# Kernel tuning notes

Measured on AMD Instinct MI355X. Metric: run time of the kernel, lower is better.

## Reference

```python
import jax, jax.numpy as jnp
import numpy as np
import math

N, E, D, H, L = 50000, 800000, 256, 8, 8
DK = D // H
DFF = 4 * D


def _layernorm(h, g, b, eps=1e-5):
    m = jnp.mean(h, axis=-1, keepdims=True)
    v = jnp.mean((h - m) ** 2, axis=-1, keepdims=True)
    return (h - m) * jax.lax.rsqrt(v + eps) * g + b


def setup_inputs() -> dict:
    key = jax.random.key(0)
    ks = jax.random.split(key, 16)
    s = 1.0 / math.sqrt(D)
    x = jax.random.normal(ks[0], (N, D), dtype=jnp.float32)
    # every node gets >=1 in-edge so z > 0 everywhere (as in real connected graphs)
    edge_src = jax.random.randint(ks[1], (E,), 0, N, dtype=jnp.int32)
    edge_dst = jnp.concatenate([
        jnp.arange(N, dtype=jnp.int32),
        jax.random.randint(ks[2], (E - N,), 0, N, dtype=jnp.int32),
    ])
    return {
        "x": x,
        "edge_src": edge_src,
        "edge_dst": edge_dst,
        "Wq": jax.random.normal(ks[3], (L, D, D), dtype=jnp.float32) * s,
        "bq": jnp.zeros((L, D), dtype=jnp.float32),
        "Wk": jax.random.normal(ks[4], (L, D, D), dtype=jnp.float32) * s,
        "Wv": jax.random.normal(ks[5], (L, D, D), dtype=jnp.float32) * s,
        "Wo": jax.random.normal(ks[6], (L, D, D), dtype=jnp.float32) * s,
        "bo": jnp.zeros((L, D), dtype=jnp.float32),
        "ln1_g": jnp.ones((L, D), dtype=jnp.float32),
        "ln1_b": jnp.zeros((L, D), dtype=jnp.float32),
        "W1": jax.random.normal(ks[7], (L, D, DFF), dtype=jnp.float32) * s,
        "b1": jnp.zeros((L, DFF), dtype=jnp.float32),
        "W2": jax.random.normal(ks[8], (L, DFF, D), dtype=jnp.float32) * (1.0 / math.sqrt(DFF)),
        "b2": jnp.zeros((L, D), dtype=jnp.float32),
        "ln2_g": jnp.ones((L, D), dtype=jnp.float32),
        "ln2_b": jnp.zeros((L, D), dtype=jnp.float32),
    }


def _layer(x, src, dst, Wq, bq, Wk, Wv, Wo, bo, g1, b1n, W1, b1, W2, b2, g2, b2n):
    n = x.shape[0]
    q = (x @ Wq + bq).reshape(n, H, DK)
    k = (x @ Wk).reshape(n, H, DK)
    v = (x @ Wv).reshape(n, H, DK)
    # edge score: src_dot_dst('k','q') -> [E, H]
    score = jnp.einsum('ehd,ehd->eh', k[src], q[dst])
    # scaled_exp: exp(clamp(score / sqrt(d_k), -5, 5))
    score = jnp.exp(jnp.clip(score / math.sqrt(DK), -5.0, 5.0))
    # u_mul_e + sum aggregation -> wv [N, H, DK]; copy_edge + sum -> z [N, H]
    msg = v[src] * score[:, :, None]
    wv = jax.ops.segment_sum(msg, dst, num_segments=n)
    z = jax.ops.segment_sum(score, dst, num_segments=n)
    o = (wv / z[:, :, None]).reshape(n, D)
    h = _layernorm(x + o @ Wo + bo, g1, b1n)
    # FFN with residual + layernorm
    ff = jax.nn.relu(h @ W1 + b1) @ W2 + b2
    return _layernorm(h + ff, g2, b2n)


def reference(x, edge_src, edge_dst, Wq, bq, Wk, Wv, Wo, bo, ln1_g, ln1_b,
              W1, b1, W2, b2, ln2_g, ln2_b):
    for i in range(L):
        x = _layer(x, edge_src, edge_dst, Wq[i], bq[i], Wk[i], Wv[i], Wo[i],
                   bo[i], ln1_g[i], ln1_b[i], W1[i], b1[i], W2[i], b2[i],
                   ln2_g[i], ln2_b[i])
    return x
```

## Files before the change

kernel.cpp:

```cpp
#include <hip/hip_runtime.h>
#include <cstdint>
#include <cstddef>

#define D 256
#define H 8
#define DFF 1024

typedef short s16x8 __attribute__((ext_vector_type(8)));
typedef float f32x4 __attribute__((ext_vector_type(4)));

static inline int cdiv(int a, int b) { return (a + b - 1) / b; }

__device__ inline uint16_t f2bf(float x) {
    unsigned u = __float_as_uint(x);
    u += 0x7FFFu + ((u >> 16) & 1u);
    return (uint16_t)(u >> 16);
}
__device__ inline float bf2f(uint16_t h) {
    return __uint_as_float(((unsigned)h) << 16);
}

__device__ inline void gload_lds16(const void* g, void* l) {
    __builtin_amdgcn_global_load_lds(
        (const __attribute__((address_space(1))) void*)g,
        (__attribute__((address_space(3))) void*)l, 16, 0, 0);
}

__global__ __launch_bounds__(256) void zero_int_kernel(int* __restrict__ p, int count)
{
    int i = blockIdx.x * blockDim.x + threadIdx.x;
    if (i < count) p[i] = 0;
}

__global__ __launch_bounds__(256) void count_deg_kernel(
    const int* __restrict__ edst, int* __restrict__ deg, int E)
{
    int e = blockIdx.x * blockDim.x + threadIdx.x;
    if (e < E) atomicAdd(&deg[edst[e]], 1);
}

__global__ __launch_bounds__(256) void block_sum_kernel(
    const int* __restrict__ deg, int* __restrict__ bsum, int N)
{
    int t = threadIdx.x;
    int gid = blockIdx.x * 256 + t;
    int val = (gid < N) ? deg[gid] : 0;
    #pragma unroll
    for (int o = 1; o < 64; o <<= 1) val += __shfl_xor(val, o);
    __shared__ int r[4];
    if ((t & 63) == 0) r[t >> 6] = val;
    __syncthreads();
    if (t == 0) bsum[blockIdx.x] = r[0] + r[1] + r[2] + r[3];
}

__global__ __launch_bounds__(256) void scan_bsum_kernel(int* __restrict__ bsum, int nb)
{
    __shared__ int tmp[256];
    int t = threadIdx.x;
    int val = (t < nb) ? bsum[t] : 0;
    tmp[t] = val;
    __syncthreads();
    for (int off = 1; off < 256; off <<= 1) {
        int add = (t >= off) ? tmp[t - off] : 0;
        __syncthreads();
        tmp[t] += add;
        __syncthreads();
    }
    if (t < nb) bsum[t] = tmp[t] - val;
}

__global__ __launch_bounds__(256) void scan_write_kernel(
    const int* __restrict__ deg, const int* __restrict__ bsum,
    int* __restrict__ rowptr, int* __restrict__ cursor, int N)
{
    __shared__ int tmp[256];
    int t = threadIdx.x;
    int gid = blockIdx.x * 256 + t;
    int val = (gid < N) ? deg[gid] : 0;
    tmp[t] = val;
    __syncthreads();
    for (int off = 1; off < 256; off <<= 1) {
        int add = (t >= off) ? tmp[t - off] : 0;
        __syncthreads();
        tmp[t] += add;
        __syncthreads();
    }
    int excl = tmp[t] - val + bsum[blockIdx.x];
    if (gid < N) { rowptr[gid] = excl; cursor[gid] = excl; }
    if (gid == N - 1) rowptr[N] = excl + val;
}

__global__ __launch_bounds__(256) void fill_csr_kernel(
    const int* __restrict__ esrc, const int* __restrict__ edst,
    int* __restrict__ cursor, int* __restrict__ csr_src, int E)
{
    int e = blockIdx.x * blockDim.x + threadIdx.x;
    if (e < E) {
        int pos = atomicAdd(&cursor[edst[e]], 1);
        csr_src[pos] = esrc[e];
    }
}

__global__ __launch_bounds__(256) void transpose_cast_kernel(
    const float* __restrict__ in, uint16_t* __restrict__ out,
    int R, int C, size_t inLS, size_t outLS)
{
    __shared__ float t[32][33];
    in  += blockIdx.z * inLS;
    out += blockIdx.z * outLS;
    int c0 = blockIdx.x * 32, r0 = blockIdx.y * 32;
    int tx = threadIdx.x, ty = threadIdx.y;
    #pragma unroll
    for (int i = 0; i < 4; ++i)
        t[ty + i * 8][tx] = in[(size_t)(r0 + ty + i * 8) * C + c0 + tx];
    __syncthreads();
    #pragma unroll
    for (int i = 0; i < 4; ++i)
        out[(size_t)(c0 + ty + i * 8) * R + r0 + tx] = f2bf(t[tx][ty + i * 8]);
}

__global__ __launch_bounds__(256) void cast_f32_bf16_kernel(
    const float* __restrict__ in, uint16_t* __restrict__ out, int n4)
{
    int i = blockIdx.x * blockDim.x + threadIdx.x;
    if (i >= n4) return;
    float4 f = ((const float4*)in)[i];
    uint16_t o0 = f2bf(f.x), o1 = f2bf(f.y), o2 = f2bf(f.z), o3 = f2bf(f.w);
    uint2 pk;
    pk.x = (unsigned)o0 | ((unsigned)o1 << 16);
    pk.y = (unsigned)o2 | ((unsigned)o3 << 16);
    ((uint2*)out)[i] = pk;
}

__global__ __launch_bounds__(256) void build_qkv_bias_kernel(
    const float* __restrict__ bq, float* __restrict__ qb, int total)
{
    int i = blockIdx.x * blockDim.x + threadIdx.x;
    if (i >= total) return;
    int l = i / 768, c = i - l * 768;
    qb[i] = (c < 256) ? bq[l * 256 + c] : 0.f;
}

__global__ __launch_bounds__(256) void gemm_bf16_kernel(
    const uint16_t* __restrict__ A, int lda, int M, int K,
    const uint16_t* __restrict__ BT, int Nc,
    const float* __restrict__ bias,
    uint16_t* __restrict__ Cb, int relu)
{
    __shared__ __align__(16) uint16_t As[128 * 32];
    __shared__ __align__(16) uint16_t Bs[128 * 32];

    const int tid  = threadIdx.x;
    const int lane = tid & 63;
    const int w    = tid >> 6;
    const int wr   = w >> 1, wc = w & 1;
    const int quad = lane >> 4;
    const int l15  = lane & 15;

    const int m0 = blockIdx.x * 128;
    const int n0 = blockIdx.y * 128;

    f32x4 acc[4][4] = {};

    const int jbase = w * 2;
    const int srow  = lane >> 2;
    const int skc   = (lane & 3) * 8;

    for (int k0 = 0; k0 < K; k0 += 32) {
        #pragma unroll
        for (int jj = 0; jj < 2; ++jj) {
            int j = jbase + jj;
            int r = j * 16 + srow;
            int gr = m0 + r; if (gr > M - 1) gr = M - 1;
            gload_lds16(A  + (size_t)gr * lda + k0 + skc, &As[j * 512]);
            gload_lds16(BT + (size_t)(n0 + r) * K + k0 + skc, &Bs[j * 512]);
        }
        __syncthreads();

        s16x8 af[4], bf[4];
        #pragma unroll
        for (int t = 0; t < 4; ++t) {
            af[t] = *(const s16x8*)&As[(wr * 64 + t * 16 + l15) * 32 + quad * 8];
            bf[t] = *(const s16x8*)&Bs[(wc * 64 + t * 16 + l15) * 32 + quad * 8];
        }
        #pragma unroll
        for (int i = 0; i < 4; ++i)
            #pragma unroll
            for (int jt = 0; jt < 4; ++jt)
                acc[i][jt] = __builtin_amdgcn_mfma_f32_16x16x32_bf16(
                    af[i], bf[jt], acc[i][jt], 0, 0, 0);
        __syncthreads();
    }

    float bv[4];
    #pragma unroll
    for (int jt = 0; jt < 4; ++jt)
        bv[jt] = bias ? bias[n0 + wc * 64 + jt * 16 + l15] : 0.f;

    #pragma unroll
    for (int i = 0; i < 4; ++i) {
        #pragma unroll
        for (int r = 0; r < 4; ++r) {
            int m = m0 + wr * 64 + i * 16 + quad * 4 + r;
            if (m >= M) continue;
            #pragma unroll
            for (int jt = 0; jt < 4; ++jt) {
                int n = n0 + wc * 64 + jt * 16 + l15;
                float val = acc[i][jt][r] + bv[jt];
                if (relu) val = fmaxf(val, 0.f);
                Cb[(size_t)m * Nc + n] = f2bf(val);
            }
        }
    }
}

__global__ __launch_bounds__(256) void gemm_ln_kernel(
    const uint16_t* __restrict__ A, int lda, int M, int K,
    const uint16_t* __restrict__ BT,
    const float* __restrict__ bias,
    const float* __restrict__ resid,
    const float* __restrict__ g, const float* __restrict__ b,
    float* __restrict__ Cf, uint16_t* __restrict__ Cb)
{
    __shared__ __align__(16) uint16_t As[64 * 32];
    __shared__ __align__(16) uint16_t Bs[256 * 32];
    __shared__ float sS[64][4];
    __shared__ float sQ[64][4];

    const int tid  = threadIdx.x;
    const int lane = tid & 63;
    const int w    = tid >> 6;
    const int quad = lane >> 4;
    const int l15  = lane & 15;

    const int m0 = blockIdx.x * 64;

    f32x4 acc[4][4] = {};

    for (int k0 = 0; k0 < K; k0 += 32) {
        {
            int slot = tid;
            int r = slot >> 2, kc = (slot & 3) * 8;
            int gr = m0 + r; if (gr > M - 1) gr = M - 1;
            gload_lds16(A + (size_t)gr * lda + k0 + kc, &As[slot * 8]);
        }
        #pragma unroll
        for (int i = 0; i < 4; ++i) {
            int slot = i * 256 + tid;
            int n = slot >> 2, kc = (slot & 3) * 8;
            gload_lds16(BT + (size_t)n * K + k0 + kc, &Bs[slot * 8]);
        }
        __syncthreads();

        s16x8 af[4], bf[4];
        #pragma unroll
        for (int t = 0; t < 4; ++t) {
            af[t] = *(const s16x8*)&As[(t * 16 + l15) * 32 + quad * 8];
            bf[t] = *(const s16x8*)&Bs[(w * 64 + t * 16 + l15) * 32 + quad * 8];
        }
        #pragma unroll
        for (int i = 0; i < 4; ++i)
            #pragma unroll
            for (int jt = 0; jt < 4; ++jt)
                acc[i][jt] = __builtin_amdgcn_mfma_f32_16x16x32_bf16(
                    af[i], bf[jt], acc[i][jt], 0, 0, 0);
        __syncthreads();
    }

    float bv[4], gv[4], bbv[4];
    #pragma unroll
    for (int jt = 0; jt < 4; ++jt) {
        int n = w * 64 + jt * 16 + l15;
        bv[jt]  = bias[n];
        gv[jt]  = g[n];
        bbv[jt] = b[n];
    }

    #pragma unroll
    for (int i = 0; i < 4; ++i) {
        #pragma unroll
        for (int r = 0; r < 4; ++r) {
            int ml = i * 16 + quad * 4 + r;
            int m  = m0 + ml;
            bool valid = (m < M);
            float s = 0.f, s2 = 0.f;
            #pragma unroll
            for (int jt = 0; jt < 4; ++jt) {
                int n = w * 64 + jt * 16 + l15;
                float val = acc[i][jt][r] + bv[jt];
                if (valid) val += resid[(size_t)m * 256 + n];
                acc[i][jt][r] = val;
                s += val;
                s2 += val * val;
            }
            #pragma unroll
            for (int o = 1; o < 16; o <<= 1) {
                s  += __shfl_xor(s, o);
                s2 += __shfl_xor(s2, o);
            }
            if (l15 == 0) { sS[ml][w] = s; sQ[ml][w] = s2; }
        }
    }
    __syncthreads();

    #pragma unroll
    for (int i = 0; i < 4; ++i) {
        #pragma unroll
        for (int r = 0; r < 4; ++r) {
            int ml = i * 16 + quad * 4 + r;
            int m  = m0 + ml;
            if (m >= M) continue;
            float s  = sS[ml][0] + sS[ml][1] + sS[ml][2] + sS[ml][3];
            float s2 = sQ[ml][0] + sQ[ml][1] + sQ[ml][2] + sQ[ml][3];
            float mean = s * (1.f / 256.f);
            float var  = s2 * (1.f / 256.f) - mean * mean;
            float rstd = rsqrtf(var + 1e-5f);
            #pragma unroll
            for (int jt = 0; jt < 4; ++jt) {
                int n = w * 64 + jt * 16 + l15;
                float out = (acc[i][jt][r] - mean) * rstd * gv[jt] + bbv[jt];
                Cf[(size_t)m * 256 + n] = out;
                if (Cb) Cb[(size_t)m * 256 + n] = f2bf(out);
            }
        }
    }
}

__global__ __launch_bounds__(256) void node_attn_kernel(
    uint16_t* __restrict__ qkv,
    const int* __restrict__ rowptr, const int* __restrict__ csr_src, int N)
{
    int node = (blockIdx.x * blockDim.x + threadIdx.x) >> 6;
    int lane = threadIdx.x & 63;
    if (node >= N) return;

    uint16_t* qp = qkv + (size_t)node * 768 + lane * 4;
    uint2 qu = *(const uint2*)qp;
    float q0 = bf2f((uint16_t)(qu.x & 0xFFFF)), q1 = bf2f((uint16_t)(qu.x >> 16));
    float q2 = bf2f((uint16_t)(qu.y & 0xFFFF)), q3 = bf2f((uint16_t)(qu.y >> 16));

    float a0 = 0.f, a1 = 0.f, a2 = 0.f, a3 = 0.f, zacc = 0.f;
    const float inv_sqrt_dk = 0.17677669529663687f;

    int beg = rowptr[node], end = rowptr[node + 1];
    int i = beg;
    for (; i + 1 < end; i += 2) {
        int s0 = csr_src[i], s1 = csr_src[i + 1];
        const uint16_t* b0 = qkv + (size_t)s0 * 768;
        const uint16_t* b1 = qkv + (size_t)s1 * 768;
        uint2 ku0 = *(const uint2*)(b0 + 256 + lane * 4);
        uint2 ku1 = *(const uint2*)(b1 + 256 + lane * 4);
        uint2 vu0 = *(const uint2*)(b0 + 512 + lane * 4);
        uint2 vu1 = *(const uint2*)(b1 + 512 + lane * 4);

        float p0 = bf2f((uint16_t)(ku0.x & 0xFFFF)) * q0
                 + bf2f((uint16_t)(ku0.x >> 16))   * q1
                 + bf2f((uint16_t)(ku0.y & 0xFFFF)) * q2
                 + bf2f((uint16_t)(ku0.y >> 16))   * q3;
        float p1 = bf2f((uint16_t)(ku1.x & 0xFFFF)) * q0
                 + bf2f((uint16_t)(ku1.x >> 16))   * q1
                 + bf2f((uint16_t)(ku1.y & 0xFFFF)) * q2
                 + bf2f((uint16_t)(ku1.y >> 16))   * q3;
        p0 += __shfl_xor(p0, 1); p1 += __shfl_xor(p1, 1);
        p0 += __shfl_xor(p0, 2); p1 += __shfl_xor(p1, 2);
        p0 += __shfl_xor(p0, 4); p1 += __shfl_xor(p1, 4);
        float sc0 = __expf(fminf(fmaxf(p0 * inv_sqrt_dk, -5.f), 5.f));
        float sc1 = __expf(fminf(fmaxf(p1 * inv_sqrt_dk, -5.f), 5.f));

        a0 += bf2f((uint16_t)(vu0.x & 0xFFFF)) * sc0;
        a1 += bf2f((uint16_t)(vu0.x >> 16))   * sc0;
        a2 += bf2f((uint16_t)(vu0.y & 0xFFFF)) * sc0;
        a3 += bf2f((uint16_t)(vu0.y >> 16))   * sc0;
        zacc += sc0;
        a0 += bf2f((uint16_t)(vu1.x & 0xFFFF)) * sc1;
        a1 += bf2f((uint16_t)(vu1.x >> 16))   * sc1;
        a2 += bf2f((uint16_t)(vu1.y & 0xFFFF)) * sc1;
        a3 += bf2f((uint16_t)(vu1.y >> 16))   * sc1;
        zacc += sc1;
    }
    if (i < end) {
        int s = csr_src[i];
        const uint16_t* base = qkv + (size_t)s * 768;
        uint2 ku = *(const uint2*)(base + 256 + lane * 4);
        float p = bf2f((uint16_t)(ku.x & 0xFFFF)) * q0
                + bf2f((uint16_t)(ku.x >> 16))   * q1
                + bf2f((uint16_t)(ku.y & 0xFFFF)) * q2
                + bf2f((uint16_t)(ku.y >> 16))   * q3;
        p += __shfl_xor(p, 1);
        p += __shfl_xor(p, 2);
        p += __shfl_xor(p, 4);
        float sc = __expf(fminf(fmaxf(p * inv_sqrt_dk, -5.f), 5.f));
        uint2 vu = *(const uint2*)(base + 512 + lane * 4);
        a0 += bf2f((uint16_t)(vu.x & 0xFFFF)) * sc;
        a1 += bf2f((uint16_t)(vu.x >> 16))   * sc;
        a2 += bf2f((uint16_t)(vu.y & 0xFFFF)) * sc;
        a3 += bf2f((uint16_t)(vu.y >> 16))   * sc;
        zacc += sc;
    }
    float inv = 1.f / zacc;
    uint2 pk;
    pk.x = (unsigned)f2bf(a0 * inv) | ((unsigned)f2bf(a1 * inv) << 16);
    pk.y = (unsigned)f2bf(a2 * inv) | ((unsigned)f2bf(a3 * inv) << 16);
    *(uint2*)qp = pk;
}

extern "C" void kernel_launch(void* const* d_in, const int* in_sizes, int n_in,
                              void* d_out, int out_size, void* d_ws, size_t ws_size,
                              hipStream_t stream)
{
    const float* x0   = (const float*)d_in[0];
    const int* esrc   = (const int*)d_in[1];
    const int* edst   = (const int*)d_in[2];
    const float* Wq   = (const float*)d_in[3];
    const float* bq   = (const float*)d_in[4];
    const float* Wk   = (const float*)d_in[5];
    const float* Wv   = (const float*)d_in[6];
    const float* Wo   = (const float*)d_in[7];
    const float* bo   = (const float*)d_in[8];
    const float* ln1g = (const float*)d_in[9];
    const float* ln1b = (const float*)d_in[10];
    const float* W1   = (const float*)d_in[11];
    const float* b1   = (const float*)d_in[12];
    const float* W2   = (const float*)d_in[13];
    const float* b2   = (const float*)d_in[14];
    const float* ln2g = (const float*)d_in[15];
    const float* ln2b = (const float*)d_in[16];

    const int N = in_sizes[0] / D;
    const int E = in_sizes[1];
    const int L = in_sizes[3] / (D * D);
    const size_t ND = (size_t)N * D;

    char* p = (char*)d_ws;
    float* bufX = (float*)p;         p += ND * 4;
    uint16_t* xb  = (uint16_t*)p;
    uint16_t* t1  = xb;              p += ND * 2;
    uint16_t* qkv = (uint16_t*)p;    p += (size_t)N * 768 * 2;
    uint16_t* hb  = (uint16_t*)p;    p += ND * 2;
    uint16_t* BTqkv = (uint16_t*)p;  p += (size_t)L * 768 * 256 * 2;
    uint16_t* BTo   = (uint16_t*)p;  p += (size_t)L * 256 * 256 * 2;
    uint16_t* BT1   = (uint16_t*)p;  p += (size_t)L * 1024 * 256 * 2;
    uint16_t* BT2   = (uint16_t*)p;  p += (size_t)L * 256 * 1024 * 2;
    float* qbias    = (float*)p;     p += (size_t)L * 768 * 4;
    int* rowptr  = (int*)p;          p += (size_t)(N + 1) * 4;
    int* cursor  = (int*)p;          p += (size_t)N * 4;
    int* deg     = cursor;
    int* csr_src = (int*)p;          p += (size_t)E * 4;
    int* bsum    = (int*)p;

    const int nb = cdiv(N, 256);
    dim3 blk(256);
    int edgeBlocks = cdiv(E, 256);
    int nodeBlocks = cdiv(N, 4);

    dim3 tb(32, 8);
    transpose_cast_kernel<<<dim3(8, 8, L), tb, 0, stream>>>(Wq, BTqkv, 256, 256, (size_t)65536, (size_t)768 * 256);
    transpose_cast_kernel<<<dim3(8, 8, L), tb, 0, stream>>>(Wk, BTqkv + 256 * 256, 256, 256, (size_t)65536, (size_t)768 * 256);
    transpose_cast_kernel<<<dim3(8, 8, L), tb, 0, stream>>>(Wv, BTqkv + 512 * 256, 256, 256, (size_t)65536, (size_t)768 * 256);
    transpose_cast_kernel<<<dim3(8, 8, L), tb, 0, stream>>>(Wo, BTo, 256, 256, (size_t)65536, (size_t)65536);
    transpose_cast_kernel<<<dim3(32, 8, L), tb, 0, stream>>>(W1, BT1, 256, 1024, (size_t)262144, (size_t)262144);
    transpose_cast_kernel<<<dim3(8, 32, L), tb, 0, stream>>>(W2, BT2, 1024, 256, (size_t)262144, (size_t)262144);
    build_qkv_bias_kernel<<<cdiv(L * 768, 256), blk, 0, stream>>>(bq, qbias, L * 768);
    cast_f32_bf16_kernel<<<cdiv((int)(ND / 4), 256), blk, 0, stream>>>(x0, xb, (int)(ND / 4));

    zero_int_kernel<<<cdiv(N, 256), blk, 0, stream>>>(deg, N);
    count_deg_kernel<<<edgeBlocks, blk, 0, stream>>>(edst, deg, E);
    block_sum_kernel<<<nb, blk, 0, stream>>>(deg, bsum, N);
    scan_bsum_kernel<<<1, blk, 0, stream>>>(bsum, nb);
    scan_write_kernel<<<nb, blk, 0, stream>>>(deg, bsum, rowptr, cursor, N);
    fill_csr_kernel<<<edgeBlocks, blk, 0, stream>>>(esrc, edst, cursor, csr_src, E);

    const int Mt128 = cdiv(N, 128);
    const int Mt64  = cdiv(N, 64);
    dim3 gQKV(Mt128, 768 / 128);
    dim3 gF1(Mt128, 1024 / 128);
    dim3 gLN(Mt64, 1);

    for (int l = 0; l < L; ++l) {
        const uint16_t* BTqkv_l = BTqkv + (size_t)l * 768 * 256;
        const uint16_t* BTo_l   = BTo + (size_t)l * 65536;
        const uint16_t* BT1_l   = BT1 + (size_t)l * 262144;
        const uint16_t* BT2_l   = BT2 + (size_t)l * 262144;
        const float* xin_f = (l == 0) ? x0 : bufX;

        gemm_bf16_kernel<<<gQKV, blk, 0, stream>>>(xb, 256, N, 256, BTqkv_l, 768,
            qbias + (size_t)l * 768, qkv, 0);

        node_attn_kernel<<<nodeBlocks, blk, 0, stream>>>(qkv, rowptr, csr_src, N);

        gemm_ln_kernel<<<gLN, blk, 0, stream>>>(qkv, 768, N, 256, BTo_l,
            bo + (size_t)l * 256, xin_f, ln1g + (size_t)l * 256, ln1b + (size_t)l * 256,
            bufX, hb);

        gemm_bf16_kernel<<<gF1, blk, 0, stream>>>(hb, 256, N, 256, BT1_l, 1024,
            b1 + (size_t)l * 1024, t1, 1);

        float* fout = (l == L - 1) ? (float*)d_out : bufX;
        gemm_ln_kernel<<<gLN, blk, 0, stream>>>(t1, 1024, N, 1024, BT2_l,
            b2 + (size_t)l * 256, bufX, ln2g + (size_t)l * 256, ln2b + (size_t)l * 256,
            fout, (l == L - 1) ? nullptr : xb);

        xin_f = bufX;
    }
}
```

Before: 3.425 ms.

## Remap GEMM tiles across XCDs and unroll edge gather loop by four

The GEMM kernel now remaps its linear workgroup index so that consecutive tiles land on the same XCD chiplet, which is meant to improve L2 reuse of shared operand tiles. The node attention kernel unrolls the edge loop from two to four gathers, giving more memory loads in flight per wave. It also uses readfirstlane to make the node and source indices wave-uniform scalars, and folds the 1/sqrt(dk) scale into q. The wider unroll raises register pressure, and the tile remap assumes round-robin dispatch across eight XCDs.

After: 3.437 ms. No clear change (+0.4%).

```diff
diff --git a/kernel.cpp b/kernel.cpp
--- a/kernel.cpp
+++ b/kernel.cpp
@@ -157,8 +157,16 @@
     const int quad = lane >> 4;
     const int l15  = lane & 15;
 
-    const int m0 = blockIdx.x * 128;
-    const int n0 = blockIdx.y * 128;
+    const int nwg = gridDim.x * gridDim.y;
+    const int lin = blockIdx.y * gridDim.x + blockIdx.x;
+    const int xcd = lin & 7, idx = lin >> 3;
+    const int q8 = nwg >> 3, r8 = nwg & 7;
+    const int lin2 = (xcd < r8 ? xcd * (q8 + 1) : r8 * (q8 + 1) + (xcd - r8) * q8) + idx;
+    const int mt = lin2 % gridDim.x;
+    const int nt = lin2 / gridDim.x;
+
+    const int m0 = mt * 128;
+    const int n0 = nt * 128;
 
     f32x4 acc[4][4] = {};
 
@@ -333,68 +341,109 @@
     int node = (blockIdx.x * blockDim.x + threadIdx.x) >> 6;
     int lane = threadIdx.x & 63;
     if (node >= N) return;
+    node = __builtin_amdgcn_readfirstlane(node);
+
+    const float inv_sqrt_dk = 0.17677669529663687f;
 
     uint16_t* qp = qkv + (size_t)node * 768 + lane * 4;
     uint2 qu = *(const uint2*)qp;
-    float q0 = bf2f((uint16_t)(qu.x & 0xFFFF)), q1 = bf2f((uint16_t)(qu.x >> 16));
-    float q2 = bf2f((uint16_t)(qu.y & 0xFFFF)), q3 = bf2f((uint16_t)(qu.y >> 16));
+    float q0 = bf2f((uint16_t)(qu.x & 0xFFFF)) * inv_sqrt_dk;
+    float q1 = bf2f((uint16_t)(qu.x >> 16))    * inv_sqrt_dk;
+    float q2 = bf2f((uint16_t)(qu.y & 0xFFFF)) * inv_sqrt_dk;
+    float q3 = bf2f((uint16_t)(qu.y >> 16))    * inv_sqrt_dk;
 
     float a0 = 0.f, a1 = 0.f, a2 = 0.f, a3 = 0.f, zacc = 0.f;
-    const float inv_sqrt_dk = 0.17677669529663687f;
+    const int voff = lane * 4;
 
     int beg = rowptr[node], end = rowptr[node + 1];
     int i = beg;
-    for (; i + 1 < end; i += 2) {
-        int s0 = csr_src[i], s1 = csr_src[i + 1];
-        const uint16_t* b0 = qkv + (size_t)s0 * 768;
-        const uint16_t* b1 = qkv + (size_t)s1 * 768;
-        uint2 ku0 = *(const uint2*)(b0 + 256 + lane * 4);
-        uint2 ku1 = *(const uint2*)(b1 + 256 + lane * 4);
-        uint2 vu0 = *(const uint2*)(b0 + 512 + lane * 4);
-        uint2 vu1 = *(const uint2*)(b1 + 512 + lane * 4);
+
+    for (; i + 3 < end; i += 4) {
+        int s0 = __builtin_amdgcn_readfirstlane(csr_src[i]);
+        int s1 = __builtin_amdgcn_readfirstlane(csr_src[i + 1]);
+        int s2 = __builtin_amdgcn_readfirstlane(csr_src[i + 2]);
+        int s3 = __builtin_amdgcn_readfirstlane(csr_src[i + 3]);
+        const uint16_t* b0 = qkv + (size_t)s0 * 768 + voff;
+        const uint16_t* b1 = qkv + (size_t)s1 * 768 + voff;
+        const uint16_t* b2 = qkv + (size_t)s2 * 768 + voff;
+        const uint16_t* b3 = qkv + (size_t)s3 * 768 + voff;
+
+        uint2 ku0 = *(const uint2*)(b0 + 256);
+        uint2 ku1 = *(const uint2*)(b1 + 256);
+        uint2 ku2 = *(const uint2*)(b2 + 256);
+        uint2 ku3 = *(const uint2*)(b3 + 256);
+        uint2 vu0 = *(const uint2*)(b0 + 512);
+        uint2 vu1 = *(const uint2*)(b1 + 512);
+        uint2 vu2 = *(const uint2*)(b2 + 512);
+        uint2 vu3 = *(const uint2*)(b3 + 512);
 
         float p0 = bf2f((uint16_t)(ku0.x & 0xFFFF)) * q0
-                 + bf2f((uint16_t)(ku0.x >> 16))   * q1
+                 + bf2f((uint16_t)(ku0.x >> 16))    * q1
                  + bf2f((uint16_t)(ku0.y & 0xFFFF)) * q2
-                 + bf2f((uint16_t)(ku0.y >> 16))   * q3;
+                 + bf2f((uint16_t)(ku0.y >> 16))    * q3;
         float p1 = bf2f((uint16_t)(ku1.x & 0xFFFF)) * q0
-                 + bf2f((uint16_t)(ku1.x >> 16))   * q1
+                 + bf2f((uint16_t)(ku1.x >> 16))    * q1
                  + bf2f((uint16_t)(ku1.y & 0xFFFF)) * q2
-                 + bf2f((uint16_t)(ku1.y >> 16))   * q3;
+                 + bf2f((uint16_t)(ku1.y >> 16))    * q3;
+        float p2 = bf2f((uint16_t)(ku2.x & 0xFFFF)) * q0
+                 + bf2f((uint16_t)(ku2.x >> 16))    * q1
+                 + bf2f((uint16_t)(ku2.y & 0xFFFF)) * q2
+                 + bf2f((uint16_t)(ku2.y >> 16))    * q3;
+        float p3 = bf2f((uint16_t)(ku3.x & 0xFFFF)) * q0
+                 + bf2f((uint16_t)(ku3.x >> 16))    * q1
+                 + bf2f((uint16_t)(ku3.y & 0xFFFF)) * q2
+                 + bf2f((uint16_t)(ku3.y >> 16))    * q3;
+
         p0 += __shfl_xor(p0, 1); p1 += __shfl_xor(p1, 1);
+        p2 += __shfl_xor(p2, 1); p3 += __shfl_xor(p3, 1);
         p0 += __shfl_xor(p0, 2); p1 += __shfl_xor(p1, 2);
+        p2 += __shfl_xor(p2, 2); p3 += __shfl_xor(p3, 2);
         p0 += __shfl_xor(p0, 4); p1 += __shfl_xor(p1, 4);
-        float sc0 = __expf(fminf(fmaxf(p0 * inv_sqrt_dk, -5.f), 5.f));
-        float sc1 = __expf(fminf(fmaxf(p1 * inv_sqrt_dk, -5.f), 5.f));
+        p2 += __shfl_xor(p2, 4); p3 += __shfl_xor(p3, 4);
+
+        float sc0 = __expf(fminf(fmaxf(p0, -5.f), 5.f));
+        float sc1 = __expf(fminf(fmaxf(p1, -5.f), 5.f));
+        float sc2 = __expf(fminf(fmaxf(p2, -5.f), 5.f));
+        float sc3 = __expf(fminf(fmaxf(p3, -5.f), 5.f));
 
         a0 += bf2f((uint16_t)(vu0.x & 0xFFFF)) * sc0;
-        a1 += bf2f((uint16_t)(vu0.x >> 16))   * sc0;
+        a1 += bf2f((uint16_t)(vu0.x >> 16))    * sc0;
         a2 += bf2f((uint16_t)(vu0.y & 0xFFFF)) * sc0;
-        a3 += bf2f((uint16_t)(vu0.y >> 16))   * sc0;
+        a3 += bf2f((uint16_t)(vu0.y >> 16))    * sc0;
         zacc += sc0;
         a0 += bf2f((uint16_t)(vu1.x & 0xFFFF)) * sc1;
-        a1 += bf2f((uint16_t)(vu1.x >> 16))   * sc1;
+        a1 += bf2f((uint16_t)(vu1.x >> 16))    * sc1;
         a2 += bf2f((uint16_t)(vu1.y & 0xFFFF)) * sc1;
-        a3 += bf2f((uint16_t)(vu1.y >> 16))   * sc1;
+        a3 += bf2f((uint16_t)(vu1.y >> 16))    * sc1;
         zacc += sc1;
-    }
-    if (i < end) {
-        int s = csr_src[i];
-        const uint16_t* base = qkv + (size_t)s * 768;
-        uint2 ku = *(const uint2*)(base + 256 + lane * 4);
+        a0 += bf2f((uint16_t)(vu2.x & 0xFFFF)) * sc2;
+        a1 += bf2f((uint16_t)(vu2.x >> 16))    * sc2;
+        a2 += bf2f((uint16_t)(vu2.y & 0xFFFF)) * sc2;
+        a3 += bf2f((uint16_t)(vu2.y >> 16))    * sc2;
+        zacc += sc2;
+        a0 += bf2f((uint16_t)(vu3.x & 0xFFFF)) * sc3;
+        a1 += bf2f((uint16_t)(vu3.x >> 16))    * sc3;
+        a2 += bf2f((uint16_t)(vu3.y & 0xFFFF)) * sc3;
+        a3 += bf2f((uint16_t)(vu3.y >> 16))    * sc3;
+        zacc += sc3;
+    }
+    for (; i < end; ++i) {
+        int s = __builtin_amdgcn_readfirstlane(csr_src[i]);
+        const uint16_t* base = qkv + (size_t)s * 768 + voff;
+        uint2 ku = *(const uint2*)(base + 256);
+        uint2 vu = *(const uint2*)(base + 512);
         float p = bf2f((uint16_t)(ku.x & 0xFFFF)) * q0
-                + bf2f((uint16_t)(ku.x >> 16))   * q1
+                + bf2f((uint16_t)(ku.x >> 16))    * q1
                 + bf2f((uint16_t)(ku.y & 0xFFFF)) * q2
-                + bf2f((uint16_t)(ku.y >> 16))   * q3;
+                + bf2f((uint16_t)(ku.y >> 16))    * q3;
         p += __shfl_xor(p, 1);
         p += __shfl_xor(p, 2);
         p += __shfl_xor(p, 4);
-        float sc = __expf(fminf(fmaxf(p * inv_sqrt_dk, -5.f), 5.f));
-        uint2 vu = *(const uint2*)(base + 512 + lane * 4);
+        float sc = __expf(fminf(fmaxf(p, -5.f), 5.f));
         a0 += bf2f((uint16_t)(vu.x & 0xFFFF)) * sc;
-        a1 += bf2f((uint16_t)(vu.x >> 16))   * sc;
+        a1 += bf2f((uint16_t)(vu.x >> 16))    * sc;
         a2 += bf2f((uint16_t)(vu.y & 0xFFFF)) * sc;
-        a3 += bf2f((uint16_t)(vu.y >> 16))   * sc;
+        a3 += bf2f((uint16_t)(vu.y >> 16))    * sc;
         zacc += sc;
     }
     float inv = 1.f / zacc;
```
